# Kernel tuning notes

Measured on AMD Instinct MI355X. Metric: run time of the kernel, lower is better.

## Reference

```python
import jax, jax.numpy as jnp
import numpy as np

B, S, UNITS = 32, 2048, 512
D = 2 * UNITS  # 1024


def setup_inputs() -> dict:
    key = jax.random.key(0)
    ks = jax.random.split(key, 12)
    s = 1.0 / np.sqrt(D)
    mask = (jax.random.uniform(ks[0], (B, S)) < 0.9).astype(jnp.float32)
    mask = mask.at[:, 0].set(1.0)  # guarantee no all-zero row
    return {
        "dec_hidden": jax.random.normal(ks[1], (2, B, UNITS), dtype=jnp.float32),
        "enc_output": jax.random.normal(ks[2], (B, S, D), dtype=jnp.float32),
        "enc_pad_mask": mask,
        "prev_coverage": jax.random.uniform(ks[3], (B, S), dtype=jnp.float32) * 0.1,
        "Wh": jax.random.uniform(ks[4], (D, D), minval=-s, maxval=s),
        "bh": jax.random.uniform(ks[5], (D,), minval=-s, maxval=s),
        "Ws": jax.random.uniform(ks[6], (D, D), minval=-s, maxval=s),
        "bs": jax.random.uniform(ks[7], (D,), minval=-s, maxval=s),
        "Wc": jax.random.uniform(ks[8], (D, 1), minval=-1.0, maxval=1.0),
        "bc": jax.random.uniform(ks[9], (D,), minval=-1.0, maxval=1.0),
        "v": jax.random.uniform(ks[10], (1, D), minval=-s, maxval=s),
        "bv": jax.random.uniform(ks[11], (1,), minval=-s, maxval=s),
        "use_coverage": 1,
    }


def reference(dec_hidden, enc_output, enc_pad_mask, prev_coverage,
              Wh, bh, Ws, bs, Wc, bc, v, bv, use_coverage):
    # dec_hidden: (2, B, units) -> (B, 1, 2*units)
    dec = jnp.transpose(dec_hidden, (1, 0, 2)).reshape(dec_hidden.shape[1], 1, -1)
    enc_features = jnp.einsum('bsd,ed->bse', enc_output, Wh) + bh  # (B,S,D)
    dec_features = jnp.einsum('bod,ed->boe', dec, Ws) + bs          # (B,1,D)
    att_inputs = enc_features + dec_features
    if use_coverage:
        # Linear(1 -> D) applied to prev_coverage[..., None]
        coverage_features = prev_coverage[:, :, None] * Wc[:, 0][None, None, :] + bc
        att_inputs = att_inputs + coverage_features
    score = jnp.einsum('bsd,od->bso', jnp.tanh(att_inputs), v) + bv  # (B,S,1)
    attention_weights = jax.nn.softmax(score, axis=1)[..., 0]        # (B,S)
    attention_weights = attention_weights * enc_pad_mask
    attention_weights = attention_weights / jnp.sum(attention_weights, axis=1, keepdims=True)
    context_vector = jnp.einsum('bs,bsd->bd', attention_weights, enc_output)
    if use_coverage:
        coverage_vector = prev_coverage + attention_weights
        return context_vector, attention_weights, coverage_vector
    return context_vector, attention_weights
```

## Files before the change

kernel.cpp:

```cpp
#include <hip/hip_runtime.h>
#include <hip/hip_bf16.h>

#define BATCH 32
#define SEQ   2048
#define DIM   1024

typedef __attribute__((ext_vector_type(4))) float f32x4;
typedef __attribute__((ext_vector_type(8))) short short8;

static __device__ __forceinline__ ushort f2bf(float x) {
    __hip_bfloat16 h = __float2bfloat16(x);
    union { __hip_bfloat16 h; ushort u; } cv; cv.h = h;
    return cv.u;
}
static __device__ __forceinline__ float bf2f(ushort u) {
    union { unsigned int i; float f; } cv; cv.i = ((unsigned int)u) << 16;
    return cv.f;
}

static __device__ __forceinline__ void gll16(const void* g, void* l) {
    __builtin_amdgcn_global_load_lds(
        (const __attribute__((address_space(1))) void*)g,
        (__attribute__((address_space(3))) void*)l, 16, 0, 0);
}

__global__ __launch_bounds__(256) void kAPack(const float* __restrict__ enc,
                                              ushort* __restrict__ apk) {
    int g = blockIdx.x * 256 + threadIdx.x;
    int lane = g & 63;
    int frag = (g >> 6) & 31;
    int kt   = (g >> 11) & 15;
    int strip = g >> 15;
    int mt = frag >> 1, kb = frag & 1;
    int row = (strip << 8) + (mt << 4) + (lane & 15);
    int k0  = (kt << 6) + (kb << 5) + ((lane >> 4) << 3);
    const float* src = enc + (size_t)row * DIM + k0;
    float4 a = *(const float4*)src;
    float4 b = *(const float4*)(src + 4);
    union { ushort us[8]; uint4 u4; } pk;
    pk.us[0] = f2bf(a.x); pk.us[1] = f2bf(a.y); pk.us[2] = f2bf(a.z); pk.us[3] = f2bf(a.w);
    pk.us[4] = f2bf(b.x); pk.us[5] = f2bf(b.y); pk.us[6] = f2bf(b.z); pk.us[7] = f2bf(b.w);
    *(uint4*)(apk + (size_t)g * 8) = pk.u4;
}

__global__ __launch_bounds__(256) void kWhPack(const float* __restrict__ Wh,
                                               ushort* __restrict__ bpk) {
    int g = blockIdx.x * 256 + threadIdx.x;
    int lane = g & 63;
    int frag = (g >> 6) & 31;
    int kt   = (g >> 11) & 15;
    int nb   = g >> 15;
    int ebl = frag >> 1, kbit = frag & 1;
    int e  = (nb << 8) + (ebl << 4) + (lane & 15);
    int k0 = (kt << 6) + (kbit << 5) + ((lane >> 4) << 3);
    const float* src = Wh + (size_t)e * DIM + k0;
    float4 a = *(const float4*)src;
    float4 b = *(const float4*)(src + 4);
    union { ushort us[8]; uint4 u4; } pk;
    pk.us[0] = f2bf(a.x); pk.us[1] = f2bf(a.y); pk.us[2] = f2bf(a.z); pk.us[3] = f2bf(a.w);
    pk.us[4] = f2bf(b.x); pk.us[5] = f2bf(b.y); pk.us[6] = f2bf(b.z); pk.us[7] = f2bf(b.w);
    *(uint4*)(bpk + (size_t)g * 8) = pk.u4;
}

__global__ __launch_bounds__(256) void kBase(const float* __restrict__ dh,
                                             const float* __restrict__ Ws,
                                             const float* __restrict__ bs,
                                             const float* __restrict__ bh,
                                             const float* __restrict__ bc,
                                             const int* __restrict__ uc,
                                             float* __restrict__ base) {
    __shared__ float dec[8][DIM];
    int ec = blockIdx.x >> 2;
    int bg = blockIdx.x & 3;
    int b0 = bg * 8, e0 = ec * 32;
    int tid = threadIdx.x;
    for (int i = tid; i < 8 * DIM; i += 256) {
        int bb = i >> 10, d = i & 1023;
        float vdec = (d < 512) ? dh[(b0 + bb) * 512 + d]
                               : dh[BATCH * 512 + (b0 + bb) * 512 + d - 512];
        dec[bb][d] = vdec;
    }
    __syncthreads();
    int el = tid >> 3, ds = tid & 7;
    int e = e0 + el;
    float acc[8] = {0.f, 0.f, 0.f, 0.f, 0.f, 0.f, 0.f, 0.f};
    const float* wrow = Ws + (size_t)e * DIM;
    for (int i = 0; i < 128; ++i) {
        int d = i * 8 + ds;
        float wv = wrow[d];
#pragma unroll
        for (int bb = 0; bb < 8; ++bb) acc[bb] += wv * dec[bb][d];
    }
#pragma unroll
    for (int bb = 0; bb < 8; ++bb) {
        float s = acc[bb];
        s += __shfl_xor(s, 1); s += __shfl_xor(s, 2); s += __shfl_xor(s, 4);
        acc[bb] = s;
    }
    if (ds == 0) {
        float bias = bs[e] + bh[e] + ((*uc) ? bc[e] : 0.0f);
#pragma unroll
        for (int bb = 0; bb < 8; ++bb) base[(b0 + bb) * DIM + e] = acc[bb] + bias;
    }
}

__global__ __launch_bounds__(256, 3) void kScore(const ushort* __restrict__ apk,
                                                 const ushort* __restrict__ bpk,
                                                 const float* __restrict__ base,
                                                 const float* __restrict__ pc,
                                                 const float* __restrict__ Wc,
                                                 const float* __restrict__ vv,
                                                 const int* __restrict__ uc,
                                                 float* __restrict__ scorep) {
    __shared__ ushort Al[2][8 * 512];
    __shared__ ushort Bl[2][8 * 512];
    __shared__ float red[2][128];

    const int tid = threadIdx.x;
    const int w = tid >> 6, lane = tid & 63;
    const int q = lane >> 4, l15 = lane & 15;
    const int wm = w >> 1, wn = w & 1;

    const int x = blockIdx.x & 7;
    const int j = blockIdx.x >> 3;
    const int ms = (x << 6) + (j >> 3);
    const int np = j & 7;
    const int b = ms >> 4;
    const int s0 = (ms & 15) << 7;

    const ushort* abase = apk + ((size_t)(ms >> 1) << 18);
    const ushort* bbase = bpk + ((size_t)(np >> 1) << 18);
    const int hM = (ms & 1) << 3;
    const int hN = (np & 1) << 3;

#define STAGE(S, BUF) do { \
    int kt_ = (S) >> 1, kb_ = (S) & 1; \
    const ushort* ak_ = abase + ((size_t)kt_ << 14); \
    const ushort* bk_ = bbase + ((size_t)kt_ << 14); \
    _Pragma("unroll") \
    for (int c_ = 0; c_ < 2; ++c_) { \
        int a_ = (w << 1) + c_; \
        gll16(ak_ + ((((hM + a_) << 1) + kb_) << 9) + (lane << 3), &Al[BUF][a_ << 9]); \
        gll16(bk_ + ((((hN + a_) << 1) + kb_) << 9) + (lane << 3), &Bl[BUF][a_ << 9]); \
    } } while (0)

    f32x4 acc[4][4] = {};

    STAGE(0, 0);
    __syncthreads();

    int buf = 0;
    for (int s = 0; s < 32; ++s) {
        if (s < 31) STAGE(s + 1, buf ^ 1);
        short8 a_[4], b_[4];
#pragma unroll
        for (int mf = 0; mf < 4; ++mf)
            a_[mf] = *(const short8*)&Al[buf][(((wm << 2) + mf) << 9) + (lane << 3)];
#pragma unroll
        for (int ef = 0; ef < 4; ++ef)
            b_[ef] = *(const short8*)&Bl[buf][(((wn << 2) + ef) << 9) + (lane << 3)];
#pragma unroll
        for (int ef = 0; ef < 4; ++ef)
#pragma unroll
            for (int mf = 0; mf < 4; ++mf)
                acc[mf][ef] = __builtin_amdgcn_mfma_f32_16x16x32_bf16(a_[mf], b_[ef], acc[mf][ef], 0, 0, 0);
        __syncthreads();
        buf ^= 1;
    }

    const float ucf = (float)(*uc);
    float basee[4], ve[4], wce[4];
#pragma unroll
    for (int ef = 0; ef < 4; ++ef) {
        int e = (np << 7) + (wn << 6) + (ef << 4) + l15;
        basee[ef] = base[b * DIM + e];
        ve[ef] = vv[e];
        wce[ef] = Wc[e] * ucf;
    }
#pragma unroll
    for (int mf = 0; mf < 4; ++mf) {
#pragma unroll
        for (int r = 0; r < 4; ++r) {
            int rl = (wm << 6) + (mf << 4) + (q << 2) + r;
            float p = pc[b * SEQ + s0 + rl];
            float sp = 0.f;
#pragma unroll
            for (int ef = 0; ef < 4; ++ef) {
                float xv = acc[mf][ef][r] + basee[ef] + p * wce[ef];
                float tt = 1.0f - 2.0f / (1.0f + __expf(2.0f * xv));
                sp += tt * ve[ef];
            }
            sp += __shfl_xor(sp, 1);
            sp += __shfl_xor(sp, 2);
            sp += __shfl_xor(sp, 4);
            sp += __shfl_xor(sp, 8);
            if (l15 == 0) red[wn][rl] = sp;
        }
    }
    __syncthreads();
    if (tid < 128)
        scorep[np * (BATCH * SEQ) + b * SEQ + s0 + tid] = red[0][tid] + red[1][tid];
}

__global__ __launch_bounds__(512) void kSoftmax(const float* __restrict__ scorep,
                                                const float* __restrict__ mask,
                                                const float* __restrict__ pc,
                                                float* __restrict__ att,
                                                float* __restrict__ cov,
                                                int write_cov) {
    __shared__ float rmax[8], rsum[8];
    const int BS = BATCH * SEQ;
    int b = blockIdx.x, tid = threadIdx.x;
    int wv = tid >> 6, ln = tid & 63;
    float x[4];
#pragma unroll
    for (int i = 0; i < 4; ++i) {
        int idx = b * SEQ + tid + i * 512;
        float s01 = scorep[idx] + scorep[BS + idx];
        float s23 = scorep[2 * BS + idx] + scorep[3 * BS + idx];
        float s45 = scorep[4 * BS + idx] + scorep[5 * BS + idx];
        float s67 = scorep[6 * BS + idx] + scorep[7 * BS + idx];
        x[i] = (s01 + s23) + (s45 + s67);
    }
    float m = fmaxf(fmaxf(x[0], x[1]), fmaxf(x[2], x[3]));
#pragma unroll
    for (int o = 1; o < 64; o <<= 1) m = fmaxf(m, __shfl_xor(m, o));
    if (ln == 0) rmax[wv] = m;
    __syncthreads();
    m = rmax[0];
#pragma unroll
    for (int i = 1; i < 8; ++i) m = fmaxf(m, rmax[i]);

    float ms[4], wm[4];
#pragma unroll
    for (int i = 0; i < 4; ++i) ms[i] = mask[b * SEQ + tid + i * 512];
    float s = 0.f;
#pragma unroll
    for (int i = 0; i < 4; ++i) { wm[i] = __expf(x[i] - m) * ms[i]; s += wm[i]; }
#pragma unroll
    for (int o = 1; o < 64; o <<= 1) s += __shfl_xor(s, o);
    if (ln == 0) rsum[wv] = s;
    __syncthreads();
    s = 0.f;
#pragma unroll
    for (int i = 0; i < 8; ++i) s += rsum[i];
    float inv = 1.0f / s;
#pragma unroll
    for (int i = 0; i < 4; ++i) {
        float wf = wm[i] * inv;
        att[b * SEQ + tid + i * 512] = wf;
        if (write_cov) cov[b * SEQ + tid + i * 512] = pc[b * SEQ + tid + i * 512] + wf;
    }
}

__global__ __launch_bounds__(256) void kCtxPart(const ushort* __restrict__ apk,
                                                const float* __restrict__ att,
                                                float* __restrict__ part) {
    __shared__ float attl[256];
    const int strip = blockIdx.x;
    const int tid = threadIdx.x;
    const int wv = tid >> 6, l = tid & 63;
    const int q = l >> 4, l15 = l & 15;
    attl[tid] = att[(strip << 8) + tid];
    __syncthreads();

    const ushort* sb = apk + ((size_t)strip << 18);
#pragma unroll
    for (int c = 0; c < 8; ++c) {
        int combo = (wv << 3) + c;
        int kt = combo >> 1, kb = combo & 1;
        const ushort* kbase = sb + ((size_t)kt << 14) + (kb << 9) + (l << 3);
        float a8[8] = {0.f, 0.f, 0.f, 0.f, 0.f, 0.f, 0.f, 0.f};
#pragma unroll
        for (int mt = 0; mt < 16; ++mt) {
            short8 v = *(const short8*)(kbase + (mt << 10));
            float wgt = attl[(mt << 4) + l15];
#pragma unroll
            for (int jj = 0; jj < 8; ++jj) a8[jj] += wgt * bf2f((ushort)v[jj]);
        }
#pragma unroll
        for (int o = 1; o < 16; o <<= 1)
#pragma unroll
            for (int jj = 0; jj < 8; ++jj) a8[jj] += __shfl_xor(a8[jj], o);
        if (l15 == 0) {
            int d0 = (kt << 6) + (kb << 5) + (q << 3);
            float* dst = part + ((size_t)strip << 10) + d0;
#pragma unroll
            for (int jj = 0; jj < 8; ++jj) dst[jj] = a8[jj];
        }
    }
}

__global__ __launch_bounds__(256) void kCtxReduce(const float* __restrict__ part,
                                                  float* __restrict__ ctx) {
    int g = blockIdx.x * 256 + threadIdx.x;
    int b = g >> 10, d = g & 1023;
    float s = 0.f;
#pragma unroll
    for (int i = 0; i < 8; ++i) s += part[((size_t)((b << 3) + i) << 10) + d];
    ctx[g] = s;
}

extern "C" void kernel_launch(void* const* d_in, const int* in_sizes, int n_in,
                              void* d_out, int out_size, void* d_ws, size_t ws_size,
                              hipStream_t stream) {
    const float* dh   = (const float*)d_in[0];
    const float* enc  = (const float*)d_in[1];
    const float* mask = (const float*)d_in[2];
    const float* pc   = (const float*)d_in[3];
    const float* Wh   = (const float*)d_in[4];
    const float* bh   = (const float*)d_in[5];
    const float* Ws   = (const float*)d_in[6];
    const float* bs   = (const float*)d_in[7];
    const float* Wc   = (const float*)d_in[8];
    const float* bc   = (const float*)d_in[9];
    const float* vv   = (const float*)d_in[10];
    const int* uc     = (const int*)d_in[12];

    float* ctx = (float*)d_out;
    float* att = ctx + BATCH * DIM;
    float* cov = att + BATCH * SEQ;
    int write_cov = (out_size >= BATCH * (DIM + 2 * SEQ)) ? 1 : 0;

    ushort* apk  = (ushort*)d_ws;
    ushort* bpk  = apk + (size_t)BATCH * SEQ * DIM;
    float* base   = (float*)(bpk + (size_t)DIM * DIM);
    float* scorep = base + BATCH * DIM;
    float* part   = scorep + 8 * BATCH * SEQ;

    kAPack<<<32768, 256, 0, stream>>>(enc, apk);
    kWhPack<<<512, 256, 0, stream>>>(Wh, bpk);
    kBase<<<128, 256, 0, stream>>>(dh, Ws, bs, bh, bc, uc, base);
    kScore<<<4096, 256, 0, stream>>>(apk, bpk, base, pc, Wc, vv, uc, scorep);
    kSoftmax<<<BATCH, 512, 0, stream>>>(scorep, mask, pc, att, cov, write_cov);
    kCtxPart<<<256, 256, 0, stream>>>(apk, att, part);
    kCtxReduce<<<128, 256, 0, stream>>>(part, ctx);
}
```

Measured before the change: 301.5 us.

## Repack bf16 tiles per k-step and unroll double-buffered MFMA loop

```diff
diff --git a/kernel.cpp b/kernel.cpp
--- a/kernel.cpp
+++ b/kernel.cpp
@@ -28,12 +28,11 @@
                                               ushort* __restrict__ apk) {
     int g = blockIdx.x * 256 + threadIdx.x;
     int lane = g & 63;
-    int frag = (g >> 6) & 31;
-    int kt   = (g >> 11) & 15;
+    int fr   = (g >> 6) & 15;
+    int S    = (g >> 10) & 31;
     int strip = g >> 15;
-    int mt = frag >> 1, kb = frag & 1;
-    int row = (strip << 8) + (mt << 4) + (lane & 15);
-    int k0  = (kt << 6) + (kb << 5) + ((lane >> 4) << 3);
+    int row = (strip << 8) + (fr << 4) + (lane & 15);
+    int k0  = (S << 5) + ((lane >> 4) << 3);
     const float* src = enc + (size_t)row * DIM + k0;
     float4 a = *(const float4*)src;
     float4 b = *(const float4*)(src + 4);
@@ -47,12 +46,11 @@
                                                ushort* __restrict__ bpk) {
     int g = blockIdx.x * 256 + threadIdx.x;
     int lane = g & 63;
-    int frag = (g >> 6) & 31;
-    int kt   = (g >> 11) & 15;
+    int fr   = (g >> 6) & 15;
+    int S    = (g >> 10) & 31;
     int nb   = g >> 15;
-    int ebl = frag >> 1, kbit = frag & 1;
-    int e  = (nb << 8) + (ebl << 4) + (lane & 15);
-    int k0 = (kt << 6) + (kbit << 5) + ((lane >> 4) << 3);
+    int e  = (nb << 8) + (fr << 4) + (lane & 15);
+    int k0 = (S << 5) + ((lane >> 4) << 3);
     const float* src = Wh + (size_t)e * DIM + k0;
     float4 a = *(const float4*)src;
     float4 b = *(const float4*)(src + 4);
@@ -104,7 +102,7 @@
     }
 }
 
-__global__ __launch_bounds__(256, 3) void kScore(const ushort* __restrict__ apk,
+__global__ __launch_bounds__(256, 4) void kScore(const ushort* __restrict__ apk,
                                                  const ushort* __restrict__ bpk,
                                                  const float* __restrict__ base,
                                                  const float* __restrict__ pc,
@@ -112,9 +110,8 @@
                                                  const float* __restrict__ vv,
                                                  const int* __restrict__ uc,
                                                  float* __restrict__ scorep) {
-    __shared__ ushort Al[2][8 * 512];
-    __shared__ ushort Bl[2][8 * 512];
-    __shared__ float red[2][128];
+    __shared__ ushort Al[2][4096];
+    __shared__ ushort Bl[2][4096];
 
     const int tid = threadIdx.x;
     const int w = tid >> 6, lane = tid & 63;
@@ -128,46 +125,51 @@
     const int b = ms >> 4;
     const int s0 = (ms & 15) << 7;
 
-    const ushort* abase = apk + ((size_t)(ms >> 1) << 18);
-    const ushort* bbase = bpk + ((size_t)(np >> 1) << 18);
-    const int hM = (ms & 1) << 3;
-    const int hN = (np & 1) << 3;
-
-#define STAGE(S, BUF) do { \
-    int kt_ = (S) >> 1, kb_ = (S) & 1; \
-    const ushort* ak_ = abase + ((size_t)kt_ << 14); \
-    const ushort* bk_ = bbase + ((size_t)kt_ << 14); \
+    const ushort* pa = apk + ((size_t)(ms >> 1) << 18)
+                     + ((size_t)(((ms & 1) << 3) + (w << 1)) << 9) + (lane << 3);
+    const ushort* pb = bpk + ((size_t)(np >> 1) << 18)
+                     + ((size_t)(((np & 1) << 3) + (w << 1)) << 9) + (lane << 3);
+    ushort* da0 = &Al[0][(w << 1) << 9];
+    ushort* da1 = &Al[1][(w << 1) << 9];
+    ushort* db0 = &Bl[0][(w << 1) << 9];
+    ushort* db1 = &Bl[1][(w << 1) << 9];
+
+#define STG(DA, DB) do { \
+    gll16(pa, (DA)); gll16(pa + 512, (DA) + 512); \
+    gll16(pb, (DB)); gll16(pb + 512, (DB) + 512); \
+    pa += 8192; pb += 8192; \
+} while (0)
+
+    f32x4 acc[4][4] = {};
+
+#define CMP(BUF) do { \
+    short8 a_[4], b_[4]; \
     _Pragma("unroll") \
-    for (int c_ = 0; c_ < 2; ++c_) { \
-        int a_ = (w << 1) + c_; \
-        gll16(ak_ + ((((hM + a_) << 1) + kb_) << 9) + (lane << 3), &Al[BUF][a_ << 9]); \
-        gll16(bk_ + ((((hN + a_) << 1) + kb_) << 9) + (lane << 3), &Bl[BUF][a_ << 9]); \
-    } } while (0)
-
-    f32x4 acc[4][4] = {};
-
-    STAGE(0, 0);
-    __syncthreads();
-
-    int buf = 0;
-    for (int s = 0; s < 32; ++s) {
-        if (s < 31) STAGE(s + 1, buf ^ 1);
-        short8 a_[4], b_[4];
-#pragma unroll
-        for (int mf = 0; mf < 4; ++mf)
-            a_[mf] = *(const short8*)&Al[buf][(((wm << 2) + mf) << 9) + (lane << 3)];
-#pragma unroll
-        for (int ef = 0; ef < 4; ++ef)
-            b_[ef] = *(const short8*)&Bl[buf][(((wn << 2) + ef) << 9) + (lane << 3)];
-#pragma unroll
-        for (int ef = 0; ef < 4; ++ef)
-#pragma unroll
-            for (int mf = 0; mf < 4; ++mf)
-                acc[mf][ef] = __builtin_amdgcn_mfma_f32_16x16x32_bf16(a_[mf], b_[ef], acc[mf][ef], 0, 0, 0);
+    for (int mf = 0; mf < 4; ++mf) \
+        a_[mf] = *(const short8*)&Al[BUF][(((wm << 2) + mf) << 9) + (lane << 3)]; \
+    _Pragma("unroll") \
+    for (int ef = 0; ef < 4; ++ef) \
+        b_[ef] = *(const short8*)&Bl[BUF][(((wn << 2) + ef) << 9) + (lane << 3)]; \
+    _Pragma("unroll") \
+    for (int ef = 0; ef < 4; ++ef) \
+        _Pragma("unroll") \
+        for (int mf = 0; mf < 4; ++mf) \
+            acc[mf][ef] = __builtin_amdgcn_mfma_f32_16x16x32_bf16(a_[mf], b_[ef], acc[mf][ef], 0, 0, 0); \
+} while (0)
+
+    STG(da0, db0);
+    __syncthreads();
+
+    for (int it = 0; it < 16; ++it) {
+        STG(da1, db1);
+        CMP(0);
         __syncthreads();
-        buf ^= 1;
-    }
-
+        if (it < 15) STG(da0, db0);
+        CMP(1);
+        __syncthreads();
+    }
+
+    float* red = (float*)&Al[0][0];
     const float ucf = (float)(*uc);
     float basee[4], ve[4], wce[4];
 #pragma unroll
@@ -194,12 +196,12 @@
             sp += __shfl_xor(sp, 2);
             sp += __shfl_xor(sp, 4);
             sp += __shfl_xor(sp, 8);
-            if (l15 == 0) red[wn][rl] = sp;
+            if (l15 == 0) red[(wn << 7) + rl] = sp;
         }
     }
     __syncthreads();
     if (tid < 128)
-        scorep[np * (BATCH * SEQ) + b * SEQ + s0 + tid] = red[0][tid] + red[1][tid];
+        scorep[np * (BATCH * SEQ) + b * SEQ + s0 + tid] = red[tid] + red[128 + tid];
 }
 
 __global__ __launch_bounds__(512) void kSoftmax(const float* __restrict__ scorep,
@@ -267,14 +269,13 @@
     const ushort* sb = apk + ((size_t)strip << 18);
 #pragma unroll
     for (int c = 0; c < 8; ++c) {
-        int combo = (wv << 3) + c;
-        int kt = combo >> 1, kb = combo & 1;
-        const ushort* kbase = sb + ((size_t)kt << 14) + (kb << 9) + (l << 3);
+        int S = (wv << 3) + c;
+        const ushort* kbase = sb + ((size_t)S << 13) + (l << 3);
         float a8[8] = {0.f, 0.f, 0.f, 0.f, 0.f, 0.f, 0.f, 0.f};
 #pragma unroll
-        for (int mt = 0; mt < 16; ++mt) {
-            short8 v = *(const short8*)(kbase + (mt << 10));
-            float wgt = attl[(mt << 4) + l15];
+        for (int fr = 0; fr < 16; ++fr) {
+            short8 v = *(const short8*)(kbase + (fr << 9));
+            float wgt = attl[(fr << 4) + l15];
 #pragma unroll
             for (int jj = 0; jj < 8; ++jj) a8[jj] += wgt * bf2f((ushort)v[jj]);
         }
@@ -283,7 +284,7 @@
 #pragma unroll
             for (int jj = 0; jj < 8; ++jj) a8[jj] += __shfl_xor(a8[jj], o);
         if (l15 == 0) {
-            int d0 = (kt << 6) + (kb << 5) + (q << 3);
+            int d0 = (S << 5) + (q << 3);
             float* dst = part + ((size_t)strip << 10) + d0;
 #pragma unroll
             for (int jj = 0; jj < 8; ++jj) dst[jj] = a8[jj];
```

After: 312.2 us. 3.6% more time.
